# Performance work log

Measured on AMD Instinct MI355X. Metric: run time of the kernel, lower is better.

Reference implementation:

```python
import jax, jax.numpy as jnp
import numpy as np

NALPHABET = 128
NEMBEDDING = 128
NSTATE = 512


def setup_inputs() -> dict:
    key = jax.random.key(0)
    k_w, k_emb, k_win, k_bin, k_wout, k_bout = jax.random.split(key, 6)
    b, t = 256, 256
    w = jax.random.randint(k_w, (b, t), 0, NALPHABET, dtype=jnp.int64)
    emb = jax.random.normal(k_emb, (NALPHABET, NEMBEDDING), dtype=jnp.float32)
    fan_in = NEMBEDDING + NSTATE
    bound_in = 1.0 / np.sqrt(fan_in)
    W_in = jax.random.uniform(k_win, (NSTATE, fan_in), jnp.float32, -bound_in, bound_in)
    b_in = jax.random.uniform(k_bin, (NSTATE,), jnp.float32, -bound_in, bound_in)
    bound_out = 1.0 / np.sqrt(NSTATE)
    W_out = jax.random.uniform(k_wout, (NALPHABET, NSTATE), jnp.float32, -bound_out, bound_out)
    b_out = jax.random.uniform(k_bout, (NALPHABET,), jnp.float32, -bound_out, bound_out)
    return {"w": w, "emb": emb, "W_in": W_in, "b_in": b_in, "W_out": W_out, "b_out": b_out}


def reference(w, emb, W_in, b_in, W_out, b_out):
    b = w.shape[0]
    nstate = W_in.shape[0]
    f = emb[w]  # (b, t, nembedding)
    # Split W_in into embedding and state blocks: cat((f_t, state)) @ W_in.T
    W_f = W_in[:, : emb.shape[1]]  # (nstate, nembedding)
    W_s = W_in[:, emb.shape[1]:]   # (nstate, nstate)
    # Precompute input contributions for all timesteps at once.
    fin = jnp.einsum("bte,ne->btn", f, W_f) + b_in  # (b, t, nstate)

    def step(state, fin_t):
        state_next = jnp.tanh(fin_t + state @ W_s.T)
        return state_next, state_next

    state0 = jnp.zeros((b, nstate), dtype=jnp.float32)
    _, states = jax.lax.scan(step, state0, jnp.swapaxes(fin, 0, 1))
    states = jnp.swapaxes(states, 0, 1)  # (b, t, nstate)
    y = jnp.einsum("btn,an->bta", states, W_out) + b_out  # (b, t, nalphabet)
    return y
```

## Files before the change

kernel.cpp:

```cpp
#include <hip/hip_runtime.h>
#include <stdint.h>
#include <math.h>

#define NALPH 128
#define NEMB  128
#define NST   512
#define BATCH 256
#define TLEN  256
#define FANIN 640

#define SDOT4(a, b, c) __builtin_amdgcn_sdot4((a), (b), (c), false)
typedef __attribute__((ext_vector_type(4))) int i32x4;

#define BAR_LDS() do {                                            \
    asm volatile("s_waitcnt lgkmcnt(0)\n\ts_barrier" ::: "memory"); \
    __builtin_amdgcn_sched_barrier(0);                            \
  } while (0)

__global__ __launch_bounds__(128) void k_tr(
    const float* __restrict__ W_in, float* __restrict__ WfT)
{
  int n = blockIdx.x, e = threadIdx.x;
  WfT[e * NST + n] = W_in[(size_t)n * FANIN + e];
}

__global__ __launch_bounds__(256) void k_prep(
    const float* __restrict__ emb, const float* __restrict__ W_in,
    const float* __restrict__ b_in, const float* __restrict__ W_out,
    const float* __restrict__ WfT,
    float* __restrict__ G, float* __restrict__ Sd,
    int* __restrict__ WoF, float* __restrict__ So,
    int* __restrict__ WsF)
{
  int bid = blockIdx.x, tid = threadIdx.x;
  if (bid < 256) {
    int tok = bid >> 1;
    int n   = ((bid & 1) << 8) + tid;
    const float* eb = emb + tok * NEMB;
    float acc = b_in[n];
#pragma unroll 8
    for (int e = 0; e < NEMB; ++e)
      acc = fmaf(eb[e], WfT[e * NST + n], acc);
    G[tok * NST + n] = acc;
  } else if (bid < 768) {
    int n = bid - 256;
    __shared__ float smax[128];
    float lw[4]; float m = 0.f;
    if (tid < 128) {
      float4 v = *(const float4*)(W_in + (size_t)n * FANIN + NEMB + tid * 4);
      lw[0] = v.x; lw[1] = v.y; lw[2] = v.z; lw[3] = v.w;
#pragma unroll
      for (int i = 0; i < 4; ++i) m = fmaxf(m, fabsf(lw[i]));
      smax[tid] = m;
    }
    __syncthreads();
    for (int s2 = 64; s2 > 0; s2 >>= 1) {
      if (tid < s2) smax[tid] = fmaxf(smax[tid], smax[tid + s2]);
      __syncthreads();
    }
    float mx = smax[0];
    if (tid < 128) {
      float r = 127.f / mx;
      uint32_t pk = 0;
#pragma unroll
      for (int i = 0; i < 4; ++i) {
        int qv = (int)rintf(lw[i] * r);
        qv = qv < -127 ? -127 : (qv > 127 ? 127 : qv);
        pk |= (uint32_t)(qv & 0xff) << (8 * i);
      }
      int kd = tid;
      int c = kd >> 4, hi = (kd >> 2) & 3, d = kd & 3;
      int lane = hi * 16 + (n & 15), nt = n >> 4;
      WsF[(((nt * 8 + c) * 64) + lane) * 4 + d] = (int)pk;
    }
    if (tid == 0) Sd[n] = mx / 16129.0f;
  } else {
    int a = bid - 768;
    __shared__ float smax[128];
    float lw[4]; float m = 0.f;
    if (tid < 128) {
      float4 v = *(const float4*)(W_out + (size_t)a * NST + tid * 4);
      lw[0] = v.x; lw[1] = v.y; lw[2] = v.z; lw[3] = v.w;
#pragma unroll
      for (int i = 0; i < 4; ++i) m = fmaxf(m, fabsf(lw[i]));
      smax[tid] = m;
    }
    __syncthreads();
    for (int s2 = 64; s2 > 0; s2 >>= 1) {
      if (tid < s2) smax[tid] = fmaxf(smax[tid], smax[tid + s2]);
      __syncthreads();
    }
    float mx = smax[0];
    if (tid < 128) {
      float r = 127.f / mx;
      uint32_t pk = 0;
#pragma unroll
      for (int i = 0; i < 4; ++i) {
        int qv = (int)rintf(lw[i] * r);
        qv = qv < -127 ? -127 : (qv > 127 ? 127 : qv);
        pk |= (uint32_t)(qv & 0xff) << (8 * i);
      }
      int kd = tid;
      int c = kd >> 4, hi = (kd >> 2) & 3, d = kd & 3;
      int lane = hi * 16 + (a & 15), ta = a >> 4;
      WoF[(((ta * 8 + c) * 64) + lane) * 4 + d] = (int)pk;
    }
    if (tid == 0) So[a] = mx / 16129.0f;
  }
}

__global__ __launch_bounds__(512, 1) void k_rec(
    const int* __restrict__ w, const float* __restrict__ G,
    const int* __restrict__ WsF, const float* __restrict__ Sd,
    signed char* __restrict__ qstates)
{
  __shared__ __align__(16) signed char qs[2][NST];
  int tid  = threadIdx.x;
  int lane = tid & 63, wv = tid >> 6;
  int l15  = lane & 15, hi = lane >> 4;
  int row  = blockIdx.x;

  const i32x4* wsf = (const i32x4*)WsF;
  i32x4 Bf[4][8];
#pragma unroll
  for (int q = 0; q < 4; ++q)
#pragma unroll
    for (int c = 0; c < 8; ++c)
      Bf[q][c] = wsf[((size_t)((wv * 4 + q) * 8 + c)) * 64 + lane];

  float dn = Sd[tid];
  const int* wr = w + row * TLEN;
  float g = G[wr[0] * NST + tid];

  qs[0][tid] = 0;
  __syncthreads();

  signed char* qrow = qstates + (size_t)row * TLEN * NST + tid;

  int p = 0;
  for (int t = 0; t < TLEN; ++t) {
    int tok_n = (t < TLEN - 1) ? wr[t + 1] : 0;
    float g_n = G[tok_n * NST + tid];

    i32x4 A[8];
#pragma unroll
    for (int c = 0; c < 8; ++c)
      A[c] = *(const i32x4*)(qs[p] + c * 64 + hi * 16);

    i32x4 acc0 = {0,0,0,0}, acc1 = {0,0,0,0}, acc2 = {0,0,0,0}, acc3 = {0,0,0,0};
#pragma unroll
    for (int c = 0; c < 8; ++c) {
      acc0 = __builtin_amdgcn_mfma_i32_16x16x64_i8(A[c], Bf[0][c], acc0, 0, 0, 0);
      acc1 = __builtin_amdgcn_mfma_i32_16x16x64_i8(A[c], Bf[1][c], acc1, 0, 0, 0);
      acc2 = __builtin_amdgcn_mfma_i32_16x16x64_i8(A[c], Bf[2][c], acc2, 0, 0, 0);
      acc3 = __builtin_amdgcn_mfma_i32_16x16x64_i8(A[c], Bf[3][c], acc3, 0, 0, 0);
    }

    int vm = (hi & 1) ? ((hi & 2) ? acc3[0] : acc1[0])
                      : ((hi & 2) ? acc2[0] : acc0[0]);

    float a = g + (float)vm * dn;
    a = fminf(fmaxf(a, -15.f), 15.f);
    float e = __expf(2.f * a);
    float s = fmaf(-2.f, __builtin_amdgcn_rcpf(e + 1.f), 1.f);
    signed char q8 = (signed char)(int)rintf(s * 127.f);
    qs[p ^ 1][tid] = q8;
    qrow[(size_t)t * NST] = q8;
    BAR_LDS();
    g = g_n;
    p ^= 1;
  }
}

__global__ __launch_bounds__(256) void k_out_mfma(
    const signed char* __restrict__ qstates, const int* __restrict__ WoF,
    const float* __restrict__ So, const float* __restrict__ b_out,
    float* __restrict__ y)
{
  __shared__ float sl[64 * 128];
  int tid = threadIdx.x;
  int lane = tid & 63, wv = tid >> 6;
  int l15 = lane & 15, hi = lane >> 4;
  size_t bt0 = (size_t)blockIdx.x * 64 + (size_t)wv * 16;

  const signed char* abase = qstates + (bt0 + l15) * NST + hi * 16;
  i32x4 A[8];
#pragma unroll
  for (int c = 0; c < 8; ++c) A[c] = *(const i32x4*)(abase + c * 64);

  const i32x4* wf = (const i32x4*)WoF;
#pragma unroll
  for (int ta = 0; ta < 8; ++ta) {
    const i32x4* bbase = wf + (size_t)ta * 8 * 64 + lane;
    i32x4 acc = {0, 0, 0, 0};
#pragma unroll
    for (int c = 0; c < 8; ++c)
      acc = __builtin_amdgcn_mfma_i32_16x16x64_i8(A[c], bbase[c * 64], acc, 0, 0, 0);
    int a = ta * 16 + l15;
    float s = So[a], b = b_out[a];
    float* slb = sl + (wv * 16 + hi * 4) * 128 + a;
#pragma unroll
    for (int r = 0; r < 4; ++r) slb[r * 128] = (float)acc[r] * s + b;
  }
  __syncthreads();

  float4* yb = (float4*)(y + (size_t)blockIdx.x * 64 * 128);
  const float4* sb = (const float4*)sl;
#pragma unroll
  for (int i = 0; i < 8; ++i) yb[i * 256 + tid] = sb[i * 256 + tid];
}

extern "C" void kernel_launch(void* const* d_in, const int* in_sizes, int n_in,
                              void* d_out, int out_size, void* d_ws, size_t ws_size,
                              hipStream_t stream) {
  const int*   w     = (const int*)d_in[0];
  const float* emb   = (const float*)d_in[1];
  const float* W_in  = (const float*)d_in[2];
  const float* b_in  = (const float*)d_in[3];
  const float* W_out = (const float*)d_in[4];
  const float* b_out = (const float*)d_in[5];
  float* y = (float*)d_out;

  char* ws = (char*)d_ws;
  float*       G       = (float*)ws;
  float*       WfT     = (float*)(ws + (256 << 10));
  float*       Sd      = (float*)(ws + (512 << 10));
  float*       So      = (float*)(ws + (640 << 10));
  int*         WoF     = (int*)(ws + (704 << 10));
  int*         WsF     = (int*)(ws + (768 << 10));
  signed char* qstates = (signed char*)(ws + (1024 << 10));

  k_tr  <<<512, 128, 0, stream>>>(W_in, WfT);
  k_prep<<<896, 256, 0, stream>>>(emb, W_in, b_in, W_out, WfT, G, Sd, WoF, So, WsF);
  k_rec <<<BATCH, 512, 0, stream>>>(w, G, WsF, Sd, qstates);
  k_out_mfma<<<BATCH * TLEN / 64, 256, 0, stream>>>(qstates, WoF, So, b_out, y);
}
```

Measured before the change: 268.5 us.

## Fuse output projection into recurrence kernel via LDS state ring buffer

Adds four extra wavefronts to the recurrence block that keep W_out fragments in registers and, every 16 timesteps, read the last 16 quantized states from a 32-slot LDS ring to compute output logits directly. This removes the int8 state round trip through global memory and the separate output kernel launch. The cost is a larger block, extra register pressure, and output MFMA work and uncoalesced scalar y stores that share the per-step barrier with the serial recurrence.

```diff
diff --git a/kernel.cpp b/kernel.cpp
--- a/kernel.cpp
+++ b/kernel.cpp
@@ -109,106 +109,128 @@
   }
 }
 
-__global__ __launch_bounds__(512, 1) void k_rec(
+#define RSTR 528
+__global__ __launch_bounds__(768, 1) void k_rec(
     const int* __restrict__ w, const float* __restrict__ G,
     const int* __restrict__ WsF, const float* __restrict__ Sd,
-    signed char* __restrict__ qstates)
+    const int* __restrict__ WoF, const float* __restrict__ So,
+    const float* __restrict__ b_out, float* __restrict__ y)
 {
-  __shared__ __align__(16) signed char qs[2][NST];
+  __shared__ __align__(16) signed char ring[32 * RSTR];
   int tid  = threadIdx.x;
   int lane = tid & 63, wv = tid >> 6;
   int l15  = lane & 15, hi = lane >> 4;
   int row  = blockIdx.x;
-
-  const i32x4* wsf = (const i32x4*)WsF;
+  const int* wr = w + row * TLEN;
+  int ow = wv - 8;
+
   i32x4 Bf[4][8];
-#pragma unroll
-  for (int q = 0; q < 4; ++q)
-#pragma unroll
-    for (int c = 0; c < 8; ++c)
-      Bf[q][c] = wsf[((size_t)((wv * 4 + q) * 8 + c)) * 64 + lane];
-
-  float dn = Sd[tid];
-  const int* wr = w + row * TLEN;
-  float g = G[wr[0] * NST + tid];
-
-  qs[0][tid] = 0;
+  float dn = 0.f, g = 0.f;
+  i32x4 Bo[2][8];
+  float so0 = 0.f, so1 = 0.f, bo0 = 0.f, bo1 = 0.f;
+
+  if (wv < 8) {
+    const i32x4* wsf = (const i32x4*)WsF;
+#pragma unroll
+    for (int q = 0; q < 4; ++q)
+#pragma unroll
+      for (int c = 0; c < 8; ++c)
+        Bf[q][c] = wsf[((size_t)((wv * 4 + q) * 8 + c)) * 64 + lane];
+    dn = Sd[tid];
+    g  = G[wr[0] * NST + tid];
+  } else {
+    const i32x4* wf = (const i32x4*)WoF;
+#pragma unroll
+    for (int c = 0; c < 8; ++c) {
+      Bo[0][c] = wf[((size_t)(((ow * 2 + 0) * 8) + c)) * 64 + lane];
+      Bo[1][c] = wf[((size_t)(((ow * 2 + 1) * 8) + c)) * 64 + lane];
+    }
+    int a0 = (ow * 2 + 0) * 16 + l15;
+    int a1 = (ow * 2 + 1) * 16 + l15;
+    so0 = So[a0]; bo0 = b_out[a0];
+    so1 = So[a1]; bo1 = b_out[a1];
+  }
+
+  if (tid < NST) ring[31 * RSTR + tid] = 0;
   __syncthreads();
 
-  signed char* qrow = qstates + (size_t)row * TLEN * NST + tid;
-
-  int p = 0;
+  float* yrow = y + (size_t)row * TLEN * NALPH;
+
   for (int t = 0; t < TLEN; ++t) {
-    int tok_n = (t < TLEN - 1) ? wr[t + 1] : 0;
-    float g_n = G[tok_n * NST + tid];
-
+    if (wv < 8) {
+      int tok_n = (t < TLEN - 1) ? wr[t + 1] : 0;
+      float g_n = G[tok_n * NST + tid];
+      const signed char* prev = ring + ((t - 1) & 31) * RSTR;
+      i32x4 A[8];
+#pragma unroll
+      for (int c = 0; c < 8; ++c)
+        A[c] = *(const i32x4*)(prev + c * 64 + hi * 16);
+      i32x4 acc0 = {0,0,0,0}, acc1 = {0,0,0,0}, acc2 = {0,0,0,0}, acc3 = {0,0,0,0};
+#pragma unroll
+      for (int c = 0; c < 8; ++c) {
+        acc0 = __builtin_amdgcn_mfma_i32_16x16x64_i8(A[c], Bf[0][c], acc0, 0, 0, 0);
+        acc1 = __builtin_amdgcn_mfma_i32_16x16x64_i8(A[c], Bf[1][c], acc1, 0, 0, 0);
+        acc2 = __builtin_amdgcn_mfma_i32_16x16x64_i8(A[c], Bf[2][c], acc2, 0, 0, 0);
+        acc3 = __builtin_amdgcn_mfma_i32_16x16x64_i8(A[c], Bf[3][c], acc3, 0, 0, 0);
+      }
+      int vm = (hi & 1) ? ((hi & 2) ? acc3[0] : acc1[0])
+                        : ((hi & 2) ? acc2[0] : acc0[0]);
+      float a = g + (float)vm * dn;
+      a = fminf(fmaxf(a, -15.f), 15.f);
+      float e = __expf(2.f * a);
+      float s = fmaf(-2.f, __builtin_amdgcn_rcpf(e + 1.f), 1.f);
+      signed char q8 = (signed char)(int)rintf(s * 127.f);
+      ring[(t & 31) * RSTR + tid] = q8;
+      g = g_n;
+    } else if ((t & 15) == 0 && t >= 16) {
+      int t0 = t - 16;
+      int cb = t0 & 31;
+      const signed char* abase = ring + (cb + l15) * RSTR + hi * 16;
+      i32x4 A[8];
+#pragma unroll
+      for (int c = 0; c < 8; ++c) A[c] = *(const i32x4*)(abase + c * 64);
+      i32x4 p0 = {0,0,0,0}, p1 = {0,0,0,0};
+#pragma unroll
+      for (int c = 0; c < 8; ++c) {
+        p0 = __builtin_amdgcn_mfma_i32_16x16x64_i8(A[c], Bo[0][c], p0, 0, 0, 0);
+        p1 = __builtin_amdgcn_mfma_i32_16x16x64_i8(A[c], Bo[1][c], p1, 0, 0, 0);
+      }
+      int a0 = (ow * 2 + 0) * 16 + l15;
+      int a1 = (ow * 2 + 1) * 16 + l15;
+#pragma unroll
+      for (int r = 0; r < 4; ++r) {
+        size_t rb = (size_t)(t0 + hi * 4 + r) * NALPH;
+        yrow[rb + a0] = (float)p0[r] * so0 + bo0;
+        yrow[rb + a1] = (float)p1[r] * so1 + bo1;
+      }
+    }
+    BAR_LDS();
+  }
+
+  if (wv >= 8) {
+    int t0 = TLEN - 16;
+    int cb = t0 & 31;
+    const signed char* abase = ring + (cb + l15) * RSTR + hi * 16;
     i32x4 A[8];
 #pragma unroll
-    for (int c = 0; c < 8; ++c)
-      A[c] = *(const i32x4*)(qs[p] + c * 64 + hi * 16);
-
-    i32x4 acc0 = {0,0,0,0}, acc1 = {0,0,0,0}, acc2 = {0,0,0,0}, acc3 = {0,0,0,0};
+    for (int c = 0; c < 8; ++c) A[c] = *(const i32x4*)(abase + c * 64);
+    i32x4 p0 = {0,0,0,0}, p1 = {0,0,0,0};
 #pragma unroll
     for (int c = 0; c < 8; ++c) {
-      acc0 = __builtin_amdgcn_mfma_i32_16x16x64_i8(A[c], Bf[0][c], acc0, 0, 0, 0);
-      acc1 = __builtin_amdgcn_mfma_i32_16x16x64_i8(A[c], Bf[1][c], acc1, 0, 0, 0);
-      acc2 = __builtin_amdgcn_mfma_i32_16x16x64_i8(A[c], Bf[2][c], acc2, 0, 0, 0);
-      acc3 = __builtin_amdgcn_mfma_i32_16x16x64_i8(A[c], Bf[3][c], acc3, 0, 0, 0);
-    }
-
-    int vm = (hi & 1) ? ((hi & 2) ? acc3[0] : acc1[0])
-                      : ((hi & 2) ? acc2[0] : acc0[0]);
-
-    float a = g + (float)vm * dn;
-    a = fminf(fmaxf(a, -15.f), 15.f);
-    float e = __expf(2.f * a);
-    float s = fmaf(-2.f, __builtin_amdgcn_rcpf(e + 1.f), 1.f);
-    signed char q8 = (signed char)(int)rintf(s * 127.f);
-    qs[p ^ 1][tid] = q8;
-    qrow[(size_t)t * NST] = q8;
-    BAR_LDS();
-    g = g_n;
-    p ^= 1;
-  }
-}
-
-__global__ __launch_bounds__(256) void k_out_mfma(
-    const signed char* __restrict__ qstates, const int* __restrict__ WoF,
-    const float* __restrict__ So, const float* __restrict__ b_out,
-    float* __restrict__ y)
-{
-  __shared__ float sl[64 * 128];
-  int tid = threadIdx.x;
-  int lane = tid & 63, wv = tid >> 6;
-  int l15 = lane & 15, hi = lane >> 4;
-  size_t bt0 = (size_t)blockIdx.x * 64 + (size_t)wv * 16;
-
-  const signed char* abase = qstates + (bt0 + l15) * NST + hi * 16;
-  i32x4 A[8];
-#pragma unroll
-  for (int c = 0; c < 8; ++c) A[c] = *(const i32x4*)(abase + c * 64);
-
-  const i32x4* wf = (const i32x4*)WoF;
-#pragma unroll
-  for (int ta = 0; ta < 8; ++ta) {
-    const i32x4* bbase = wf + (size_t)ta * 8 * 64 + lane;
-    i32x4 acc = {0, 0, 0, 0};
-#pragma unroll
-    for (int c = 0; c < 8; ++c)
-      acc = __builtin_amdgcn_mfma_i32_16x16x64_i8(A[c], bbase[c * 64], acc, 0, 0, 0);
-    int a = ta * 16 + l15;
-    float s = So[a], b = b_out[a];
-    float* slb = sl + (wv * 16 + hi * 4) * 128 + a;
-#pragma unroll
-    for (int r = 0; r < 4; ++r) slb[r * 128] = (float)acc[r] * s + b;
-  }
-  __syncthreads();
-
-  float4* yb = (float4*)(y + (size_t)blockIdx.x * 64 * 128);
-  const float4* sb = (const float4*)sl;
-#pragma unroll
-  for (int i = 0; i < 8; ++i) yb[i * 256 + tid] = sb[i * 256 + tid];
-}
+      p0 = __builtin_amdgcn_mfma_i32_16x16x64_i8(A[c], Bo[0][c], p0, 0, 0, 0);
+      p1 = __builtin_amdgcn_mfma_i32_16x16x64_i8(A[c], Bo[1][c], p1, 0, 0, 0);
+    }
+    int a0 = (ow * 2 + 0) * 16 + l15;
+    int a1 = (ow * 2 + 1) * 16 + l15;
+#pragma unroll
+    for (int r = 0; r < 4; ++r) {
+      size_t rb = (size_t)(t0 + hi * 4 + r) * NALPH;
+      yrow[rb + a0] = (float)p0[r] * so0 + bo0;
+      yrow[rb + a1] = (float)p1[r] * so1 + bo1;
+    }
+  }
+}
+#undef RSTR
 
 extern "C" void kernel_launch(void* const* d_in, const int* in_sizes, int n_in,
                               void* d_out, int out_size, void* d_ws, size_t ws_size,
@@ -228,10 +250,8 @@
   float*       So      = (float*)(ws + (640 << 10));
   int*         WoF     = (int*)(ws + (704 << 10));
   int*         WsF     = (int*)(ws + (768 << 10));
-  signed char* qstates = (signed char*)(ws + (1024 << 10));
 
   k_tr  <<<512, 128, 0, stream>>>(W_in, WfT);
   k_prep<<<896, 256, 0, stream>>>(emb, W_in, b_in, W_out, WfT, G, Sd, WoF, So, WsF);
-  k_rec <<<BATCH, 512, 0, stream>>>(w, G, WsF, Sd, qstates);
-  k_out_mfma<<<BATCH * TLEN / 64, 256, 0, stream>>>(qstates, WoF, So, b_out, y);
-}
+  k_rec <<<BATCH, 768, 0, stream>>>(w, G, WsF, Sd, WoF, So, b_out, y);
+}
```

Result: slower. 316.4 us (+17.8%).
